# Optimization experiments

Measured on AMD Instinct MI355X. Metric: run time of the kernel, lower is better.

## Reference

```python
import jax, jax.numpy as jnp
import numpy as np

NUM_CLASSES = 5  # original computes int(mask.max())+1 at runtime; labels are drawn in [0,5) so this is 5.
EPS = 1e-07


def setup_inputs() -> dict:
    key = jax.random.key(0)
    k1, k2 = jax.random.split(key)
    output = jax.random.randint(k1, (128, 1, 512, 512), 0, NUM_CLASSES).astype(jnp.float32)
    mask = jax.random.randint(k2, (1, 128, 512, 512), 0, NUM_CLASSES).astype(jnp.int32)
    return {"output": output, "mask": mask}


def reference(output, mask):
    # Squeeze to [D, H, W] volumes, as the torch module does.
    p = jnp.squeeze(output, 1)          # [D, H, W] float labels
    m = jnp.squeeze(mask, 0)            # [D, H, W] int labels

    pi = p.astype(jnp.int32).ravel()    # predicted class per voxel
    mi = m.ravel()                      # target class per voxel

    ones = jnp.ones(pi.shape, dtype=jnp.float32)
    # den1[i] = sum((p==i)^2) = count of voxels predicted i  (single pass histogram)
    den1 = jax.ops.segment_sum(ones, pi, num_segments=NUM_CLASSES)
    # den2[i] = count of voxels labeled i
    den2 = jax.ops.segment_sum(ones, mi, num_segments=NUM_CLASSES)
    # num[i]  = count of voxels where prediction == label == i
    agree = (pi == mi).astype(jnp.float32)
    num = jax.ops.segment_sum(agree, pi, num_segments=NUM_CLASSES)

    dice = 2.0 * ((num + EPS) / (den1 + den2 + EPS))   # [NUM_CLASSES]
    return jnp.sum(dice) / NUM_CLASSES
```

## Files before the change

kernel.cpp:

```cpp
#include <hip/hip_runtime.h>

#define NC 5
#define DICE_EPS 1e-7f

typedef unsigned long long u64;
typedef unsigned int u32;


__global__ __launch_bounds__(256) void dice_hist_kernel(
    const float* __restrict__ pred_f, const int* __restrict__ mask,
    u32* __restrict__ cnt, int n)
{
    u32 den1[NC] = {0, 0, 0, 0, 0};
    u32 den2[NC] = {0, 0, 0, 0, 0};
    u32 num [NC] = {0, 0, 0, 0, 0};

    const int nt  = gridDim.x * blockDim.x;
    const int tid = blockIdx.x * blockDim.x + threadIdx.x;
    const int n4  = n >> 2;

    const float4* __restrict__ p4 = (const float4*)pred_f;
    const int4*   __restrict__ m4 = (const int4*)mask;

    int i = tid;
    while (i < n4) {
        u64 A1 = 0, A2 = 0, AN = 0;
        for (int c = 0; c < 60 && i < n4; ++c, i += nt) {
            float4 pf = p4[i];
            int4   mv = m4[i];
            int p0 = (int)pf.x, p1 = (int)pf.y, p2 = (int)pf.z, p3 = (int)pf.w;
            int s0 = p0 << 3, s1 = p1 << 3, s2 = p2 << 3, s3 = p3 << 3;

            A1 += (1ull << s0) + (1ull << s1) + (1ull << s2) + (1ull << s3);
            A2 += (1ull << (mv.x << 3)) + (1ull << (mv.y << 3)) +
                  (1ull << (mv.z << 3)) + (1ull << (mv.w << 3));
            AN += (1ull << (p0 == mv.x ? s0 : 40)) +
                  (1ull << (p1 == mv.y ? s1 : 40)) +
                  (1ull << (p2 == mv.z ? s2 : 40)) +
                  (1ull << (p3 == mv.w ? s3 : 40));
        }
        #pragma unroll
        for (int c = 0; c < NC; ++c) {
            den1[c] += (u32)(A1 >> (8 * c)) & 0xFF;
            den2[c] += (u32)(A2 >> (8 * c)) & 0xFF;
            num [c] += (u32)(AN >> (8 * c)) & 0xFF;
        }
    }

    for (int j = (n4 << 2) + tid; j < n; j += nt) {
        int p = (int)pred_f[j];
        int m = mask[j];
        #pragma unroll
        for (int c = 0; c < NC; ++c) {
            u32 a = (p == c), b = (m == c);
            den1[c] += a;
            den2[c] += b;
            num [c] += a & b;
        }
    }

    #pragma unroll
    for (int c = 0; c < NC; ++c) {
        #pragma unroll
        for (int off = 32; off > 0; off >>= 1) {
            den1[c] += __shfl_xor(den1[c], off, 64);
            den2[c] += __shfl_xor(den2[c], off, 64);
            num [c] += __shfl_xor(num [c], off, 64);
        }
    }

    __shared__ u32 s_cnt[3 * NC];
    if (threadIdx.x < 3 * NC) s_cnt[threadIdx.x] = 0;
    __syncthreads();

    const int lane = threadIdx.x & 63;
    if (lane == 0) {
        #pragma unroll
        for (int c = 0; c < NC; ++c) {
            atomicAdd(&s_cnt[c],          den1[c]);
            atomicAdd(&s_cnt[NC + c],     den2[c]);
            atomicAdd(&s_cnt[2 * NC + c], num [c]);
        }
    }
    __syncthreads();

    if (threadIdx.x < 3 * NC) {
        atomicAdd(&cnt[threadIdx.x * 16], s_cnt[threadIdx.x]);
    }
}

__global__ void dice_final_kernel(const u32* __restrict__ cnt,
                                  float* __restrict__ out)
{
    if (blockIdx.x == 0 && threadIdx.x == 0) {
        float s = 0.0f;
        #pragma unroll
        for (int c = 0; c < NC; ++c) {
            float d1 = (float)cnt[c * 16];
            float d2 = (float)cnt[(NC + c) * 16];
            float nm = (float)cnt[(2 * NC + c) * 16];
            s += 2.0f * ((nm + DICE_EPS) / (d1 + d2 + DICE_EPS));
        }
        out[0] = s / (float)NC;
    }
}

extern "C" void kernel_launch(void* const* d_in, const int* in_sizes, int n_in,
                              void* d_out, int out_size, void* d_ws, size_t ws_size,
                              hipStream_t stream) {
    const float* pred = (const float*)d_in[0];
    const int*   mask = (const int*)d_in[1];
    const int n = in_sizes[0];

    u32* cnt = (u32*)d_ws;
    hipMemsetAsync(d_ws, 0, 3 * NC * 16 * sizeof(u32), stream);

    const int threads = 256;
    const int blocks = 2048;
    dice_hist_kernel<<<blocks, threads, 0, stream>>>(pred, mask, cnt, n);
    dice_final_kernel<<<1, 64, 0, stream>>>(cnt, (float*)d_out);
}
```

Baseline: 292.5 us.

## Unroll loads four-deep and fuse finalization via last-block ticket

The main loop now issues four independent float4/int4 loads per iteration so more memory requests are in flight per thread. Byte-packed counters are flushed on a running count rather than at a fixed inner-loop boundary. The separate finalize kernel is removed: each block takes a ticket from a global atomic, and the last block computes the dice score, which saves a kernel launch. The cost is an extra threadfence, an extra atomic per block and more register pressure from the unrolled loads.

```diff
diff --git a/kernel.cpp b/kernel.cpp
--- a/kernel.cpp
+++ b/kernel.cpp
@@ -7,9 +7,34 @@
 typedef unsigned int u32;
 
 
+__device__ __forceinline__ void accum4(float4 pf, int4 mv,
+                                       u64& A1, u64& A2, u64& AN)
+{
+    int p0 = (int)pf.x, p1 = (int)pf.y, p2 = (int)pf.z, p3 = (int)pf.w;
+    int s0 = p0 << 3, s1 = p1 << 3, s2 = p2 << 3, s3 = p3 << 3;
+    A1 += (1ull << s0) + (1ull << s1) + (1ull << s2) + (1ull << s3);
+    A2 += (1ull << (mv.x << 3)) + (1ull << (mv.y << 3)) +
+          (1ull << (mv.z << 3)) + (1ull << (mv.w << 3));
+    AN += (1ull << (p0 == mv.x ? s0 : 40)) +
+          (1ull << (p1 == mv.y ? s1 : 40)) +
+          (1ull << (p2 == mv.z ? s2 : 40)) +
+          (1ull << (p3 == mv.w ? s3 : 40));
+}
+
+#define FLUSH()                                                         \
+    do {                                                                \
+        _Pragma("unroll")                                               \
+        for (int c = 0; c < NC; ++c) {                                  \
+            den1[c] += (u32)(A1 >> (8 * c)) & 0xFF;                     \
+            den2[c] += (u32)(A2 >> (8 * c)) & 0xFF;                     \
+            num [c] += (u32)(AN >> (8 * c)) & 0xFF;                     \
+        }                                                               \
+        A1 = 0; A2 = 0; AN = 0;                                         \
+    } while (0)
+
 __global__ __launch_bounds__(256) void dice_hist_kernel(
     const float* __restrict__ pred_f, const int* __restrict__ mask,
-    u32* __restrict__ cnt, int n)
+    u32* __restrict__ cnt, float* __restrict__ out, int n, int nblocks)
 {
     u32 den1[NC] = {0, 0, 0, 0, 0};
     u32 den2[NC] = {0, 0, 0, 0, 0};
@@ -22,30 +47,32 @@
     const float4* __restrict__ p4 = (const float4*)pred_f;
     const int4*   __restrict__ m4 = (const int4*)mask;
 
+    u64 A1 = 0, A2 = 0, AN = 0;
+    int cin = 0;
+
     int i = tid;
-    while (i < n4) {
-        u64 A1 = 0, A2 = 0, AN = 0;
-        for (int c = 0; c < 60 && i < n4; ++c, i += nt) {
-            float4 pf = p4[i];
-            int4   mv = m4[i];
-            int p0 = (int)pf.x, p1 = (int)pf.y, p2 = (int)pf.z, p3 = (int)pf.w;
-            int s0 = p0 << 3, s1 = p1 << 3, s2 = p2 << 3, s3 = p3 << 3;
-
-            A1 += (1ull << s0) + (1ull << s1) + (1ull << s2) + (1ull << s3);
-            A2 += (1ull << (mv.x << 3)) + (1ull << (mv.y << 3)) +
-                  (1ull << (mv.z << 3)) + (1ull << (mv.w << 3));
-            AN += (1ull << (p0 == mv.x ? s0 : 40)) +
-                  (1ull << (p1 == mv.y ? s1 : 40)) +
-                  (1ull << (p2 == mv.z ? s2 : 40)) +
-                  (1ull << (p3 == mv.w ? s3 : 40));
-        }
-        #pragma unroll
-        for (int c = 0; c < NC; ++c) {
-            den1[c] += (u32)(A1 >> (8 * c)) & 0xFF;
-            den2[c] += (u32)(A2 >> (8 * c)) & 0xFF;
-            num [c] += (u32)(AN >> (8 * c)) & 0xFF;
-        }
+    for (; i + 3 * nt < n4; i += 4 * nt) {
+        float4 a0 = p4[i];
+        float4 a1 = p4[i + nt];
+        float4 a2 = p4[i + 2 * nt];
+        float4 a3 = p4[i + 3 * nt];
+        int4   b0 = m4[i];
+        int4   b1 = m4[i + nt];
+        int4   b2 = m4[i + 2 * nt];
+        int4   b3 = m4[i + 3 * nt];
+        accum4(a0, b0, A1, A2, AN);
+        accum4(a1, b1, A1, A2, AN);
+        accum4(a2, b2, A1, A2, AN);
+        accum4(a3, b3, A1, A2, AN);
+        cin += 16;
+        if (cin >= 224) { FLUSH(); cin = 0; }
     }
+    for (; i < n4; i += nt) {
+        accum4(p4[i], m4[i], A1, A2, AN);
+        cin += 4;
+        if (cin >= 224) { FLUSH(); cin = 0; }
+    }
+    FLUSH();
 
     for (int j = (n4 << 2) + tid; j < n; j += nt) {
         int p = (int)pred_f[j];
@@ -87,18 +114,19 @@
     if (threadIdx.x < 3 * NC) {
         atomicAdd(&cnt[threadIdx.x * 16], s_cnt[threadIdx.x]);
     }
-}
+    __threadfence();
+    __syncthreads();
 
-__global__ void dice_final_kernel(const u32* __restrict__ cnt,
-                                  float* __restrict__ out)
-{
-    if (blockIdx.x == 0 && threadIdx.x == 0) {
+    __shared__ u32 ticket;
+    if (threadIdx.x == 0) ticket = atomicAdd(&cnt[240], 1u);
+    __syncthreads();
+    if (ticket == (u32)(nblocks - 1) && threadIdx.x == 0) {
         float s = 0.0f;
         #pragma unroll
         for (int c = 0; c < NC; ++c) {
-            float d1 = (float)cnt[c * 16];
-            float d2 = (float)cnt[(NC + c) * 16];
-            float nm = (float)cnt[(2 * NC + c) * 16];
+            float d1 = (float)atomicAdd(&cnt[c * 16], 0u);
+            float d2 = (float)atomicAdd(&cnt[(NC + c) * 16], 0u);
+            float nm = (float)atomicAdd(&cnt[(2 * NC + c) * 16], 0u);
             s += 2.0f * ((nm + DICE_EPS) / (d1 + d2 + DICE_EPS));
         }
         out[0] = s / (float)NC;
@@ -113,10 +141,10 @@
     const int n = in_sizes[0];
 
     u32* cnt = (u32*)d_ws;
-    hipMemsetAsync(d_ws, 0, 3 * NC * 16 * sizeof(u32), stream);
+    hipMemsetAsync(d_ws, 0, 256 * sizeof(u32), stream);
 
     const int threads = 256;
     const int blocks = 2048;
-    dice_hist_kernel<<<blocks, threads, 0, stream>>>(pred, mask, cnt, n);
-    dice_final_kernel<<<1, 64, 0, stream>>>(cnt, (float*)d_out);
+    dice_hist_kernel<<<blocks, threads, 0, stream>>>(pred, mask, cnt,
+                                                     (float*)d_out, n, blocks);
 }
```

Measured after the change: 626.7 us. 2.14x slower.
